# Performance work log

Hardware: AMD Instinct MI355X
Metric: run time of the kernel (lower is better)

The kernel has to match this reference:

```python
import jax, jax.numpy as jnp
import numpy as np

N, E, Q, D, R, K, L = 30000, 250000, 150000, 200, 400, 50, 2
ALPHA = 0.8   # TRIPLE_QUAL_WEIGHT
BN_EPS = 1e-5


def _rotate(h, r):
    # RotatE-style composition: complex mult with (re, im) = (first half, second half)
    hr, hi = jnp.split(h, 2, axis=-1)
    rr, ri = jnp.split(r, 2, axis=-1)
    return jnp.concatenate([hr * rr - hi * ri, hr * ri + hi * rr], axis=-1)


def _bn(x, g, b):
    # BatchNorm1d in training mode (batch statistics, biased variance)
    mu = x.mean(0)
    var = x.var(0)
    return g * (x - mu) * jax.lax.rsqrt(var + BN_EPS) + b


def _lrga(x, w, b):
    # LowRankAttention: shared Linear(d,4k)+ReLU then low-rank global attention
    t = jax.nn.relu(x @ w.T + b)                 # [N, 4K]
    U, V, Z, T = t[:, :K], t[:, K:2 * K], t[:, 2 * K:3 * K], t[:, 3 * K:]
    # joint_normalize2: scalar D = 1 / (sum(U @ (V^T @ 1)) / N + 1e-6)
    nf = jnp.sum(U @ (V.T @ jnp.ones((x.shape[0], 1), x.dtype))) / x.shape[0] + 1e-6
    return jnp.concatenate([(U @ (V.T @ Z)) / nf, T], axis=1)   # [N, 2K]


def _conv(x, rel, ei, et, qr, qe, qx, p):
    # StarEConvLayer forward (sparse qual mode, OPN=QUAL_OPN=rotate, no attention/bias)
    w_in, w_out, w_loop, w_rel, w_q, loop_rel, g, b = p
    n = x.shape[0]
    rel_all = jnp.concatenate([rel, loop_rel[None, :]], axis=0)  # [2R+2, d]

    def direction(idx, etype, qr_h, qe_h, qx_h, w):
        row, col = idx[0], idx[1]   # flow=target_to_source: gather col, scatter row
        deg = jax.ops.segment_sum(jnp.ones(row.shape, x.dtype), row, num_segments=n)
        dinv = jnp.where(deg > 0, deg ** -0.5, 0.0)
        norm = dinv[row] * dinv[col]
        # qualifier update of relation embedding per edge
        q_emb = _rotate(x[qe_h], rel_all[qr_h])                      # [Qh, d]
        q_edge = jax.ops.segment_sum(q_emb, qx_h, num_segments=E) @ w_q
        rel_e = ALPHA * rel_all[etype] + (1.0 - ALPHA) * q_edge     # [E, d]
        msg = (_rotate(x[col], rel_e) @ w) * norm[:, None]
        return jax.ops.segment_sum(msg, row, num_segments=n)

    in_res = direction(ei[:, :E], et[:E], qr[:Q], qe[:Q], qx[:Q], w_in)
    out_res = direction(ei[:, E:], et[E:], qr[Q:], qe[Q:], qx[Q:], w_out)
    loop_res = _rotate(x, rel_all[-1]) @ w_loop
    out = _bn((in_res + out_res + loop_res) / 3.0, g, b)
    return jax.nn.relu(out), (rel_all @ w_rel)[:-1]


def reference(edge_index, edge_type, quals_rel, quals_ent, quals_edge,
              ent_emb, init_rel, loop_rel, w_in, w_out, w_loop, w_rel, w_q,
              conv_gamma, conv_beta, lrga_w, lrga_b, dimred_w, dimred_b,
              fuse_gamma, fuse_beta):
    rev = jnp.stack([edge_index[1], edge_index[0]])
    ei = jnp.concatenate([edge_index, rev], axis=1)        # [2, 2E]
    et = jnp.concatenate([edge_type, edge_type + R])       # [2E]
    qr = jnp.concatenate([quals_rel, quals_rel])
    qe = jnp.concatenate([quals_ent, quals_ent])
    qx = jnp.concatenate([quals_edge, quals_edge])
    x, r = ent_emb, init_rel
    for i in range(L):
        p = (w_in[i], w_out[i], w_loop[i], w_rel[i], w_q[i], loop_rel[i],
             conv_gamma[i], conv_beta[i])
        x_local, r = _conv(x, r, ei, et, qr, qe, qx, p)
        x_global = _lrga(x, lrga_w[i], lrga_b[i])
        h = jnp.concatenate([x_global, x_local, x], axis=1) @ dimred_w[i].T + dimred_b[i]
        if i < L - 1:
            x = _bn(jax.nn.relu(h), fuse_gamma, fuse_beta)
        else:
            x = h
    return x, r


def setup_inputs():
    key = jax.random.key(0)
    ks = jax.random.split(key, 16)
    s = 1.0 / np.sqrt(D)
    return {
        "edge_index": jax.random.randint(ks[0], (2, E), 0, N, dtype=jnp.int32),
        "edge_type": jax.random.randint(ks[1], (E,), 0, R, dtype=jnp.int32),
        "quals_rel": jax.random.randint(ks[2], (Q,), 0, 2 * R, dtype=jnp.int32),
        "quals_ent": jax.random.randint(ks[3], (Q,), 0, N, dtype=jnp.int32),
        "quals_edge": jax.random.randint(ks[4], (Q,), 0, E, dtype=jnp.int32),
        "ent_emb": jax.random.normal(ks[5], (N, D)) * s,
        "init_rel": jax.random.normal(ks[6], (2 * R + 1, D)) * s,
        "loop_rel": jax.random.normal(ks[7], (L, D)) * s,
        "w_in": jax.random.normal(ks[8], (L, D, D)) * s,
        "w_out": jax.random.normal(ks[9], (L, D, D)) * s,
        "w_loop": jax.random.normal(ks[10], (L, D, D)) * s,
        "w_rel": jax.random.normal(ks[11], (L, D, D)) * s,
        "w_q": jax.random.normal(ks[12], (L, D, D)) * s,
        "conv_gamma": jnp.ones((L, D)),
        "conv_beta": jnp.zeros((L, D)),
        "lrga_w": jax.random.normal(ks[13], (L, 4 * K, D)) * s,
        "lrga_b": jnp.zeros((L, 4 * K)),
        "dimred_w": jax.random.normal(ks[14], (L, D, 2 * K + 2 * D)) * (1.0 / np.sqrt(2 * K + 2 * D)),
        "dimred_b": jnp.zeros((L, D)),
        "fuse_gamma": jnp.ones((D,)),
        "fuse_beta": jnp.zeros((D,)),
    }
```

## Files before the change

### kernel.cpp

```cpp
#include <hip/hip_runtime.h>
#include <cstdint>
#include <cstddef>

#define NN      30000
#define NE      250000
#define NQ      150000
#define DIM     200
#define DH      100
#define RRR     400
#define RELROWS 801
#define RELALL  802
#define ALPHA_C 0.8f
#define BN_EPS_C 1e-5f

__global__ void hist_kernel(const int* __restrict__ idx, int n, int* __restrict__ cnt) {
    int i = blockIdx.x * blockDim.x + threadIdx.x;
    if (i < n) atomicAdd(&cnt[idx[i]], 1);
}

#define SC_BLK 256
#define SC_PER 16
#define SC_TILE (SC_BLK * SC_PER)

__global__ __launch_bounds__(SC_BLK) void scan_blocks_kernel(
    const int* __restrict__ in, int n, int* __restrict__ out, int* __restrict__ partials)
{
    __shared__ int sh[SC_BLK];
    int b = blockIdx.x, tid = threadIdx.x;
    long base = (long)b * SC_TILE + (long)tid * SC_PER;
    int loc[SC_PER];
    int s = 0;
    #pragma unroll
    for (int j = 0; j < SC_PER; ++j) {
        long idx = base + j;
        int v = (idx < n) ? in[idx] : 0;
        loc[j] = s; s += v;
    }
    sh[tid] = s;
    __syncthreads();
    for (int o = 1; o < SC_BLK; o <<= 1) {
        int t = (tid >= o) ? sh[tid - o] : 0;
        __syncthreads();
        sh[tid] += t;
        __syncthreads();
    }
    int excl = sh[tid] - s;
    #pragma unroll
    for (int j = 0; j < SC_PER; ++j) {
        long idx = base + j;
        if (idx < n) out[idx] = excl + loc[j];
    }
    if (tid == SC_BLK - 1) partials[b] = sh[tid];
}

__global__ __launch_bounds__(1024) void scan_partials_kernel(
    int* __restrict__ partials, int np, int* __restrict__ out_total)
{
    __shared__ int sh[1024];
    int tid = threadIdx.x;
    int v = (tid < np) ? partials[tid] : 0;
    sh[tid] = v;
    __syncthreads();
    for (int o = 1; o < 1024; o <<= 1) {
        int t = (tid >= o) ? sh[tid - o] : 0;
        __syncthreads();
        sh[tid] += t;
        __syncthreads();
    }
    if (tid < np) partials[tid] = sh[tid] - v;
    if (tid == 1023) out_total[0] = sh[1023];
}

__global__ __launch_bounds__(SC_BLK) void scan_add_kernel(
    int* __restrict__ out, int n, const int* __restrict__ partials)
{
    int b = blockIdx.x;
    int add = partials[b];
    long base = (long)b * SC_TILE + threadIdx.x;
    #pragma unroll
    for (int j = 0; j < SC_PER; ++j) {
        long idx = base + (long)j * SC_BLK;
        if (idx < n) out[idx] += add;
    }
}

static inline void run_exscan(const int* in, int* out, int n, int* partials, hipStream_t s) {
    int nb = (n + SC_TILE - 1) / SC_TILE;
    scan_blocks_kernel<<<nb, SC_BLK, 0, s>>>(in, n, out, partials);
    scan_partials_kernel<<<1, 1024, 0, s>>>(partials, nb, out + n);
    scan_add_kernel<<<nb, SC_BLK, 0, s>>>(out, n, partials);
}

__global__ void scatter_kernel(const int* __restrict__ rows, int* __restrict__ cur,
                               int* __restrict__ list, int n) {
    int i = blockIdx.x * blockDim.x + threadIdx.x;
    if (i < n) {
        int r = rows[i];
        int pos = atomicAdd(&cur[r], 1);
        list[pos] = i;
    }
}

__global__ void dinv_kernel(const int* __restrict__ cnt, float* __restrict__ dinv, int n) {
    int i = blockIdx.x * blockDim.x + threadIdx.x;
    if (i < n) {
        int c = cnt[i];
        dinv[i] = (c > 0) ? 1.0f / sqrtf((float)c) : 0.0f;
    }
}

__global__ void assign_kernel(const int* __restrict__ qcnt, int* __restrict__ qidx,
                              int* __restrict__ elist, int* __restrict__ nq) {
    int e = blockIdx.x * blockDim.x + threadIdx.x;
    if (e < NE) {
        if (qcnt[e] > 0) {
            int s = atomicAdd(nq, 1);
            qidx[e] = s;
            elist[s] = e;
        } else {
            qidx[e] = -1;
        }
    }
}

__global__ __launch_bounds__(256) void qual_agg_kernel(
    const float* __restrict__ x, const float* __restrict__ rel_all,
    const int* __restrict__ qptr, const int* __restrict__ qlist,
    const int* __restrict__ qrel, const int* __restrict__ qent,
    const int* __restrict__ elist, const int* __restrict__ nq,
    float* __restrict__ qsum_c)
{
    int slot = blockIdx.x * 4 + (threadIdx.x >> 6);
    if (slot >= nq[0]) return;
    int e = elist[slot];
    int lane = threadIdx.x & 63;
    int p0 = lane;
    int p1 = lane + 64;
    bool has1 = (p1 < DH);
    float ar0 = 0.f, ai0 = 0.f, ar1 = 0.f, ai1 = 0.f;
    int s = qptr[e], t = qptr[e + 1];
    for (int i = s; i < t; ++i) {
        int q = qlist[i];
        int ent = qent[q];
        int rel = qrel[q];
        const float* xr = x + (long)ent * DIM;
        const float* rp = rel_all + (long)rel * DIM;
        {
            float hr = xr[p0], hi = xr[p0 + DH];
            float rr = rp[p0], ri = rp[p0 + DH];
            ar0 += hr * rr - hi * ri;
            ai0 += hr * ri + hi * rr;
        }
        if (has1) {
            float hr = xr[p1], hi = xr[p1 + DH];
            float rr = rp[p1], ri = rp[p1 + DH];
            ar1 += hr * rr - hi * ri;
            ai1 += hr * ri + hi * rr;
        }
    }
    float* o = qsum_c + (long)slot * DIM;
    o[p0] = ar0; o[p0 + DH] = ai0;
    if (has1) { o[p1] = ar1; o[p1 + DH] = ai1; }
}

__global__ __launch_bounds__(256) void edge_agg_kernel(
    const float* __restrict__ x, const float* __restrict__ rel_all,
    const float* __restrict__ q_edge_c, const int* __restrict__ qidx,
    const int* __restrict__ ptr, const int* __restrict__ list,
    const int* __restrict__ other, const int* __restrict__ etype,
    const float* __restrict__ dinv, int rel_off,
    float* __restrict__ out, int ldo, int col_off)
{
    int n = blockIdx.x * 4 + (threadIdx.x >> 6);
    if (n >= NN) return;
    int lane = threadIdx.x & 63;
    int p0 = lane;
    int p1 = lane + 64;
    bool has1 = (p1 < DH);
    float ar0 = 0.f, ai0 = 0.f, ar1 = 0.f, ai1 = 0.f;
    int s = ptr[n], e = ptr[n + 1];
    float dn = dinv[n];
    for (int i = s; i < e; ++i) {
        int eid = list[i];
        int col = other[eid];
        int t = etype[eid] + rel_off;
        int qi = qidx[eid];
        float norm = dn * dinv[col];
        const float* xr = x + (long)col * DIM;
        const float* rp = rel_all + (long)t * DIM;
        {
            float hr = xr[p0], hi = xr[p0 + DH];
            float wr = ALPHA_C * rp[p0];
            float wi = ALPHA_C * rp[p0 + DH];
            if (qi >= 0) {
                const float* qp = q_edge_c + (long)qi * DIM;
                wr += qp[p0]; wi += qp[p0 + DH];
            }
            ar0 += (hr * wr - hi * wi) * norm;
            ai0 += (hr * wi + hi * wr) * norm;
        }
        if (has1) {
            float hr = xr[p1], hi = xr[p1 + DH];
            float wr = ALPHA_C * rp[p1];
            float wi = ALPHA_C * rp[p1 + DH];
            if (qi >= 0) {
                const float* qp = q_edge_c + (long)qi * DIM;
                wr += qp[p1]; wi += qp[p1 + DH];
            }
            ar1 += (hr * wr - hi * wi) * norm;
            ai1 += (hr * wi + hi * wr) * norm;
        }
    }
    float* o = out + (long)n * ldo + col_off;
    o[p0] = ar0; o[p0 + DH] = ai0;
    if (has1) { o[p1] = ar1; o[p1 + DH] = ai1; }
}

__global__ __launch_bounds__(256) void rot_loop_kernel(
    const float* __restrict__ x, const float* __restrict__ rel_all,
    float* __restrict__ out, int ldo, int col_off)
{
    int n = blockIdx.x * 4 + (threadIdx.x >> 6);
    if (n >= NN) return;
    int lane = threadIdx.x & 63;
    const float* rp = rel_all + (long)(RELALL - 1) * DIM;
    const float* xr = x + (long)n * DIM;
    float* o = out + (long)n * ldo + col_off;
    {
        float hr = xr[lane], hi = xr[lane + DH];
        float rr = rp[lane], ri = rp[lane + DH];
        o[lane] = hr * rr - hi * ri;
        o[lane + DH] = hr * ri + hi * rr;
    }
    int p1 = lane + 64;
    if (p1 < DH) {
        float hr = xr[p1], hi = xr[p1 + DH];
        float rr = rp[p1], ri = rp[p1 + DH];
        o[p1] = hr * rr - hi * ri;
        o[p1 + DH] = hr * ri + hi * rr;
    }
}

__global__ void zero_kernel(float* __restrict__ p, long n) {
    long i = (long)blockIdx.x * blockDim.x + threadIdx.x;
    if (i < n) p[i] = 0.f;
}

#define BM 128
#define BN 128
#define BK 16

template <bool TRANSB>
__global__ __launch_bounds__(256) void gemm_kernel(
    const float* __restrict__ A, const float* __restrict__ B, float* __restrict__ C,
    int M, int K, int Ncols, int ldc,
    float scale, const float* __restrict__ bias, int relu, int acc,
    const int* __restrict__ Mdev)
{
    int Meff = Mdev ? Mdev[0] : M;
    int row0 = blockIdx.y * BM;
    if (row0 >= Meff) return;
    int col0 = blockIdx.x * BN;
    __shared__ float As[BK][BM + 4];
    __shared__ float Bs[BK][BN + 4];
    int tid = threadIdx.x;
    int tm = tid >> 4;
    int tn = tid & 15;
    float accv[8][8] = {{0.f}};
    int ktiles = (K + BK - 1) / BK;
    for (int kt = 0; kt < ktiles; ++kt) {
        int k0 = kt * BK;
        #pragma unroll
        for (int i = 0; i < 2; ++i) {
            int f4 = tid + i * 256;
            int m  = f4 >> 2;
            int kq = (f4 & 3) * 4;
            int gm = row0 + m, gk = k0 + kq;
            float4 v = make_float4(0.f, 0.f, 0.f, 0.f);
            if (gm < Meff) {
                if (gk + 3 < K) {
                    v = *reinterpret_cast<const float4*>(A + (long)gm * K + gk);
                } else {
                    float t0[4] = {0.f, 0.f, 0.f, 0.f};
                    #pragma unroll
                    for (int j = 0; j < 4; ++j) if (gk + j < K) t0[j] = A[(long)gm * K + gk + j];
                    v = make_float4(t0[0], t0[1], t0[2], t0[3]);
                }
            }
            As[kq + 0][m] = v.x; As[kq + 1][m] = v.y; As[kq + 2][m] = v.z; As[kq + 3][m] = v.w;
        }
        if (!TRANSB) {
            #pragma unroll
            for (int i = 0; i < 2; ++i) {
                int f4 = tid + i * 256;
                int k  = f4 >> 5;
                int n4 = (f4 & 31) * 4;
                int gk = k0 + k, gn = col0 + n4;
                float4 v = make_float4(0.f, 0.f, 0.f, 0.f);
                if (gk < K) {
                    if (gn + 3 < Ncols) {
                        v = *reinterpret_cast<const float4*>(B + (long)gk * Ncols + gn);
                    } else {
                        float t0[4] = {0.f, 0.f, 0.f, 0.f};
                        #pragma unroll
                        for (int j = 0; j < 4; ++j) if (gn + j < Ncols) t0[j] = B[(long)gk * Ncols + gn + j];
                        v = make_float4(t0[0], t0[1], t0[2], t0[3]);
                    }
                }
                Bs[k][n4 + 0] = v.x; Bs[k][n4 + 1] = v.y; Bs[k][n4 + 2] = v.z; Bs[k][n4 + 3] = v.w;
            }
        } else {
            #pragma unroll
            for (int i = 0; i < 2; ++i) {
                int f4 = tid + i * 256;
                int n  = f4 >> 2;
                int kq = (f4 & 3) * 4;
                int gn = col0 + n, gk = k0 + kq;
                float4 v = make_float4(0.f, 0.f, 0.f, 0.f);
                if (gn < Ncols) {
                    if (gk + 3 < K) {
                        v = *reinterpret_cast<const float4*>(B + (long)gn * K + gk);
                    } else {
                        float t0[4] = {0.f, 0.f, 0.f, 0.f};
                        #pragma unroll
                        for (int j = 0; j < 4; ++j) if (gk + j < K) t0[j] = B[(long)gn * K + gk + j];
                        v = make_float4(t0[0], t0[1], t0[2], t0[3]);
                    }
                }
                Bs[kq + 0][n] = v.x; Bs[kq + 1][n] = v.y; Bs[kq + 2][n] = v.z; Bs[kq + 3][n] = v.w;
            }
        }
        __syncthreads();
        #pragma unroll
        for (int k = 0; k < BK; ++k) {
            float a[8], b[8];
            #pragma unroll
            for (int i = 0; i < 8; ++i) a[i] = As[k][tm * 8 + i];
            #pragma unroll
            for (int j = 0; j < 8; ++j) b[j] = Bs[k][tn * 8 + j];
            #pragma unroll
            for (int i = 0; i < 8; ++i)
                #pragma unroll
                for (int j = 0; j < 8; ++j)
                    accv[i][j] += a[i] * b[j];
        }
        __syncthreads();
    }
    #pragma unroll
    for (int i = 0; i < 8; ++i) {
        int gm = row0 + tm * 8 + i;
        if (gm >= Meff) continue;
        #pragma unroll
        for (int j = 0; j < 8; ++j) {
            int gn = col0 + tn * 8 + j;
            if (gn >= Ncols) continue;
            float v = accv[i][j] * scale;
            if (bias) v += bias[gn];
            if (relu) v = fmaxf(v, 0.f);
            long off = (long)gm * ldc + gn;
            if (acc) v += C[off];
            C[off] = v;
        }
    }
}

__global__ __launch_bounds__(256) void bn_stats_kernel(
    const float* __restrict__ in, float scale, int relu_in,
    float* __restrict__ s1, float* __restrict__ s2)
{
    int d = threadIdx.x;
    if (d >= DIM) return;
    float a = 0.f, b = 0.f;
    for (int r = blockIdx.x; r < NN; r += gridDim.x) {
        float v = in[(long)r * DIM + d] * scale;
        if (relu_in) v = fmaxf(v, 0.f);
        a += v;
        b += v * v;
    }
    atomicAdd(&s1[d], a);
    atomicAdd(&s2[d], b);
}

__global__ void bn_finalize_kernel(
    const float* __restrict__ s1, const float* __restrict__ s2,
    const float* __restrict__ g, const float* __restrict__ be,
    float* __restrict__ aa, float* __restrict__ cc)
{
    int d = threadIdx.x;
    if (d >= DIM) return;
    float mu = s1[d] / (float)NN;
    float var = s2[d] / (float)NN - mu * mu;
    float inv = 1.0f / sqrtf(var + BN_EPS_C);
    float a = g[d] * inv;
    aa[d] = a;
    cc[d] = be[d] - mu * a;
}

__global__ __launch_bounds__(256) void bn_apply_kernel(
    const float* __restrict__ in, float scale, int relu_in,
    const float* __restrict__ aa, const float* __restrict__ cc, int relu_out,
    float* __restrict__ out, int ldo, int col0)
{
    int d = threadIdx.x;
    if (d >= DIM) return;
    int r = blockIdx.x;
    float v = in[(long)r * DIM + d] * scale;
    if (relu_in) v = fmaxf(v, 0.f);
    v = aa[d] * v + cc[d];
    if (relu_out) v = fmaxf(v, 0.f);
    out[(long)r * ldo + col0 + d] = v;
}

__global__ __launch_bounds__(128) void colsum_uv_kernel(
    const float* __restrict__ t, float* __restrict__ cs)
{
    int d = threadIdx.x;
    if (d >= 100) return;
    float s = 0.f;
    for (int r = blockIdx.x; r < NN; r += gridDim.x) s += t[(long)r * DIM + d];
    atomicAdd(&cs[d], s);
}

__global__ void nf_kernel(const float* __restrict__ cs, float* __restrict__ nf) {
    int lane = threadIdx.x;
    float v = (lane < 50) ? cs[lane] * cs[50 + lane] : 0.f;
    for (int off = 32; off > 0; off >>= 1) v += __shfl_down(v, off);
    if (lane == 0) nf[0] = v / (float)NN + 1e-6f;
}

__global__ __launch_bounds__(256) void vtz_kernel(
    const float* __restrict__ t, float* __restrict__ M50)
{
    __shared__ float vz[100];
    int tid = threadIdx.x;
    float acc[10];
    #pragma unroll
    for (int a = 0; a < 10; ++a) acc[a] = 0.f;
    for (int r = blockIdx.x; r < NN; r += gridDim.x) {
        if (tid < 100) vz[tid] = t[(long)r * DIM + 50 + tid];
        __syncthreads();
        #pragma unroll
        for (int a = 0; a < 10; ++a) {
            int p = tid + a * 256;
            if (p < 2500) {
                int i = p / 50, j = p % 50;
                acc[a] += vz[i] * vz[50 + j];
            }
        }
        __syncthreads();
    }
    #pragma unroll
    for (int a = 0; a < 10; ++a) {
        int p = tid + a * 256;
        if (p < 2500) atomicAdd(&M50[p], acc[a]);
    }
}

__global__ __launch_bounds__(256) void um_kernel(
    const float* __restrict__ t, const float* __restrict__ M50,
    const float* __restrict__ nf, float* __restrict__ cat)
{
    __shared__ float Ms[2500];
    int tid = threadIdx.x;
    for (int i = tid; i < 2500; i += 256) Ms[i] = M50[i];
    __syncthreads();
    int n = blockIdx.x * 256 + tid;
    if (n >= NN) return;
    float inv = 1.0f / nf[0];
    float acc[50];
    #pragma unroll
    for (int j = 0; j < 50; ++j) acc[j] = 0.f;
    for (int k = 0; k < 50; ++k) {
        float u = t[(long)n * DIM + k];
        #pragma unroll
        for (int j = 0; j < 50; ++j) acc[j] += u * Ms[k * 50 + j];
    }
    #pragma unroll
    for (int j = 0; j < 50; ++j) cat[(long)n * 500 + j] = acc[j] * inv;
}

__global__ __launch_bounds__(256) void copy_cols_kernel(
    const float* __restrict__ src, int lds_, int sc0,
    float* __restrict__ dst, int ldd, int dc0,
    int rows, int cols)
{
    int i = blockIdx.x * blockDim.x + threadIdx.x;
    int total = rows * cols;
    if (i >= total) return;
    int r = i / cols, c = i % cols;
    dst[(long)r * ldd + dc0 + c] = src[(long)r * lds_ + sc0 + c];
}

static inline void launch_gemm(bool transB, const float* A, const float* B, float* C,
                               int Mmax, int K, int Ncols, int ldc, float scale,
                               const float* bias, int relu, int acc,
                               const int* Mdev, hipStream_t s)
{
    dim3 grid((Ncols + BN - 1) / BN, (Mmax + BM - 1) / BM);
    if (transB)
        gemm_kernel<true><<<grid, 256, 0, s>>>(A, B, C, Mmax, K, Ncols, ldc, scale, bias, relu, acc, Mdev);
    else
        gemm_kernel<false><<<grid, 256, 0, s>>>(A, B, C, Mmax, K, Ncols, ldc, scale, bias, relu, acc, Mdev);
}

extern "C" void kernel_launch(void* const* d_in, const int* in_sizes, int n_in,
                              void* d_out, int out_size, void* d_ws, size_t ws_size,
                              hipStream_t stream)
{
    const int*   edge_index = (const int*)d_in[0];
    const int*   ei0        = edge_index;
    const int*   ei1        = edge_index + NE;
    const int*   edge_type  = (const int*)d_in[1];
    const int*   quals_rel  = (const int*)d_in[2];
    const int*   quals_ent  = (const int*)d_in[3];
    const int*   quals_edge = (const int*)d_in[4];
    const float* ent_emb    = (const float*)d_in[5];
    const float* init_rel   = (const float*)d_in[6];
    const float* loop_rel   = (const float*)d_in[7];
    const float* w_in       = (const float*)d_in[8];
    const float* w_out      = (const float*)d_in[9];
    const float* w_loop     = (const float*)d_in[10];
    const float* w_rel      = (const float*)d_in[11];
    const float* w_q        = (const float*)d_in[12];
    const float* conv_gamma = (const float*)d_in[13];
    const float* conv_beta  = (const float*)d_in[14];
    const float* lrga_w     = (const float*)d_in[15];
    const float* lrga_b     = (const float*)d_in[16];
    const float* dimred_w   = (const float*)d_in[17];
    const float* dimred_b   = (const float*)d_in[18];
    const float* fuse_gamma = (const float*)d_in[19];
    const float* fuse_beta  = (const float*)d_in[20];

    float* out_x = (float*)d_out;
    float* out_r = (float*)d_out + (long)NN * DIM;

    char* wp = (char*)d_ws;
    auto alloc = [&](size_t bytes) -> void* {
        void* p = (void*)wp;
        wp += (bytes + 255) & ~(size_t)255;
        return p;
    };
    float* regionA  = (float*)alloc(sizeof(float) * (size_t)NQ * DIM);
    float* qsum_c   = regionA;
    float* pre3     = regionA;
    float* conv_sum = regionA + (size_t)NN * 600;
    float* tbuf     = conv_sum + (size_t)NN * DIM;
    float* regionB  = (float*)alloc(sizeof(float) * (size_t)NQ * DIM);
    float* q_edge_c = regionB;
    float* cat      = regionB;
    float* hbuf     = cat + (size_t)NN * 500;
    float* x_cur    = out_x;
    float* rel_all  = (float*)alloc(sizeof(float) * (size_t)RELALL * DIM);
    float* r_buf    = (float*)alloc(sizeof(float) * (size_t)RELROWS * DIM);
    float* wcat     = (float*)alloc(sizeof(float) * 600 * DIM);
    float* dinv0    = (float*)alloc(sizeof(float) * NN);
    float* dinv1    = (float*)alloc(sizeof(float) * NN);
    float* s1       = (float*)alloc(sizeof(float) * DIM);
    float* s2       = (float*)alloc(sizeof(float) * DIM);
    float* aa       = (float*)alloc(sizeof(float) * DIM);
    float* cc       = (float*)alloc(sizeof(float) * DIM);
    float* csUV     = (float*)alloc(sizeof(float) * 100);
    float* nfv      = (float*)alloc(sizeof(float) * 1);
    float* M50      = (float*)alloc(sizeof(float) * 2500);
    int* cnt0  = (int*)alloc(sizeof(int) * NN);
    int* ptr0  = (int*)alloc(sizeof(int) * (NN + 1));
    int* cur0  = (int*)alloc(sizeof(int) * NN);
    int* list0 = (int*)alloc(sizeof(int) * NE);
    int* cnt1  = (int*)alloc(sizeof(int) * NN);
    int* ptr1  = (int*)alloc(sizeof(int) * (NN + 1));
    int* cur1  = (int*)alloc(sizeof(int) * NN);
    int* list1 = (int*)alloc(sizeof(int) * NE);
    int* qcnt  = (int*)alloc(sizeof(int) * NE);
    int* qptr  = (int*)alloc(sizeof(int) * (NE + 1));
    int* qcur  = (int*)alloc(sizeof(int) * NE);
    int* qlist = (int*)alloc(sizeof(int) * NQ);
    int* qidx  = (int*)alloc(sizeof(int) * NE);
    int* elist = (int*)alloc(sizeof(int) * NQ);
    int* nq    = (int*)alloc(sizeof(int) * 1);
    int* partials = (int*)alloc(sizeof(int) * 1024);

    size_t needed = (size_t)(wp - (char*)d_ws);
    if (needed > ws_size) {
        long total_out = (long)out_size;
        zero_kernel<<<(int)((total_out + 255) / 256), 256, 0, stream>>>((float*)d_out, total_out);
        return;
    }

    hipMemsetAsync(cnt0, 0, sizeof(int) * NN, stream);
    hipMemsetAsync(cnt1, 0, sizeof(int) * NN, stream);
    hipMemsetAsync(qcnt, 0, sizeof(int) * NE, stream);
    hipMemsetAsync(nq, 0, sizeof(int), stream);
    hist_kernel<<<(NE + 255) / 256, 256, 0, stream>>>(ei0, NE, cnt0);
    hist_kernel<<<(NE + 255) / 256, 256, 0, stream>>>(ei1, NE, cnt1);
    hist_kernel<<<(NQ + 255) / 256, 256, 0, stream>>>(quals_edge, NQ, qcnt);
    run_exscan(cnt0, ptr0, NN, partials, stream);
    run_exscan(cnt1, ptr1, NN, partials, stream);
    run_exscan(qcnt, qptr, NE, partials, stream);
    hipMemcpyAsync(cur0, ptr0, sizeof(int) * NN, hipMemcpyDeviceToDevice, stream);
    hipMemcpyAsync(cur1, ptr1, sizeof(int) * NN, hipMemcpyDeviceToDevice, stream);
    hipMemcpyAsync(qcur, qptr, sizeof(int) * NE, hipMemcpyDeviceToDevice, stream);
    scatter_kernel<<<(NE + 255) / 256, 256, 0, stream>>>(ei0, cur0, list0, NE);
    scatter_kernel<<<(NE + 255) / 256, 256, 0, stream>>>(ei1, cur1, list1, NE);
    scatter_kernel<<<(NQ + 255) / 256, 256, 0, stream>>>(quals_edge, qcur, qlist, NQ);
    dinv_kernel<<<(NN + 255) / 256, 256, 0, stream>>>(cnt0, dinv0, NN);
    dinv_kernel<<<(NN + 255) / 256, 256, 0, stream>>>(cnt1, dinv1, NN);
    assign_kernel<<<(NE + 255) / 256, 256, 0, stream>>>(qcnt, qidx, elist, nq);

    for (int i = 0; i < 2; ++i) {
        const float* xin  = (i == 0) ? ent_emb : x_cur;
        const float* rsrc = (i == 0) ? init_rel : r_buf;

        hipMemcpyAsync(rel_all, rsrc, sizeof(float) * RELROWS * DIM,
                       hipMemcpyDeviceToDevice, stream);
        hipMemcpyAsync(rel_all + (long)RELROWS * DIM, loop_rel + (long)i * DIM,
                       sizeof(float) * DIM, hipMemcpyDeviceToDevice, stream);

        qual_agg_kernel<<<(NQ + 3) / 4, 256, 0, stream>>>(xin, rel_all, qptr, qlist,
                                               quals_rel, quals_ent, elist, nq, qsum_c);
        launch_gemm(false, qsum_c, w_q + (long)i * DIM * DIM, q_edge_c,
                    NQ, DIM, DIM, DIM, 1.0f - ALPHA_C, nullptr, 0, 0, nq, stream);

        edge_agg_kernel<<<(NN + 3) / 4, 256, 0, stream>>>(xin, rel_all, q_edge_c, qidx,
                                               ptr0, list0, ei1, edge_type, dinv0, 0,
                                               pre3, 600, 0);
        edge_agg_kernel<<<(NN + 3) / 4, 256, 0, stream>>>(xin, rel_all, q_edge_c, qidx,
                                               ptr1, list1, ei0, edge_type, dinv1, RRR,
                                               pre3, 600, 200);
        rot_loop_kernel<<<(NN + 3) / 4, 256, 0, stream>>>(xin, rel_all, pre3, 600, 400);

        hipMemcpyAsync(wcat,                 w_in   + (long)i * DIM * DIM, sizeof(float) * DIM * DIM, hipMemcpyDeviceToDevice, stream);
        hipMemcpyAsync(wcat + DIM * DIM,     w_out  + (long)i * DIM * DIM, sizeof(float) * DIM * DIM, hipMemcpyDeviceToDevice, stream);
        hipMemcpyAsync(wcat + 2 * DIM * DIM, w_loop + (long)i * DIM * DIM, sizeof(float) * DIM * DIM, hipMemcpyDeviceToDevice, stream);
        launch_gemm(false, pre3, wcat, conv_sum, NN, 600, DIM, DIM, 1.f, nullptr, 0, 0, nullptr, stream);

        hipMemsetAsync(s1, 0, sizeof(float) * DIM, stream);
        hipMemsetAsync(s2, 0, sizeof(float) * DIM, stream);
        bn_stats_kernel<<<512, 256, 0, stream>>>(conv_sum, 1.0f / 3.0f, 0, s1, s2);
        bn_finalize_kernel<<<1, 256, 0, stream>>>(s1, s2, conv_gamma + (long)i * DIM,
                                                  conv_beta + (long)i * DIM, aa, cc);
        bn_apply_kernel<<<NN, 256, 0, stream>>>(conv_sum, 1.0f / 3.0f, 0, aa, cc, 1,
                                                cat, 500, 100);

        launch_gemm(true, xin, lrga_w + (long)i * 200 * DIM, tbuf,
                    NN, DIM, 200, 200, 1.f, lrga_b + (long)i * 200, 1, 0, nullptr, stream);
        hipMemsetAsync(csUV, 0, sizeof(float) * 100, stream);
        hipMemsetAsync(M50, 0, sizeof(float) * 2500, stream);
        colsum_uv_kernel<<<256, 128, 0, stream>>>(tbuf, csUV);
        nf_kernel<<<1, 64, 0, stream>>>(csUV, nfv);
        vtz_kernel<<<128, 256, 0, stream>>>(tbuf, M50);
        um_kernel<<<(NN + 255) / 256, 256, 0, stream>>>(tbuf, M50, nfv, cat);
        copy_cols_kernel<<<(NN * 50 + 255) / 256, 256, 0, stream>>>(
            tbuf, DIM, 150, cat, 500, 50, NN, 50);
        copy_cols_kernel<<<(NN * DIM + 255) / 256, 256, 0, stream>>>(
            xin, DIM, 0, cat, 500, 300, NN, DIM);

        float* hdst = (i == 0) ? hbuf : out_x;
        launch_gemm(true, cat, dimred_w + (long)i * DIM * 500, hdst,
                    NN, 500, DIM, DIM, 1.f, dimred_b + (long)i * DIM, 0, 0, nullptr, stream);

        if (i == 0) {
            hipMemsetAsync(s1, 0, sizeof(float) * DIM, stream);
            hipMemsetAsync(s2, 0, sizeof(float) * DIM, stream);
            bn_stats_kernel<<<512, 256, 0, stream>>>(hdst, 1.0f, 1, s1, s2);
            bn_finalize_kernel<<<1, 256, 0, stream>>>(s1, s2, fuse_gamma, fuse_beta, aa, cc);
            bn_apply_kernel<<<NN, 256, 0, stream>>>(hdst, 1.0f, 1, aa, cc, 0,
                                                    x_cur, DIM, 0);
        }

        float* rdst = (i == 0) ? r_buf : out_r;
        launch_gemm(false, rel_all, w_rel + (long)i * DIM * DIM, rdst,
                    RELROWS, DIM, DIM, DIM, 1.f, nullptr, 0, 0, nullptr, stream);
    }
}
```

Before: 2.529 ms.

## Double-buffer GEMM shared-memory tiles and vectorize LDS fragment reads

The FP32 SIMT GEMM now keeps two shared-memory buffers per operand. The next K-tile is prefetched into registers while the current tile is computed, which drops one barrier per iteration. The thread-to-output mapping changes to two strided 4-wide fragments, so each k-step reads shared memory with four float4 loads and fewer bank conflicts. This doubles LDS use and raises register pressure, which may reduce occupancy.

New measurement: 3.098 ms. 1.22x slower.

```diff
diff --git a/kernel.cpp b/kernel.cpp
--- a/kernel.cpp
+++ b/kernel.cpp
@@ -261,14 +261,17 @@
     int row0 = blockIdx.y * BM;
     if (row0 >= Meff) return;
     int col0 = blockIdx.x * BN;
-    __shared__ float As[BK][BM + 4];
-    __shared__ float Bs[BK][BN + 4];
+    __shared__ float As[2][BK][BM + 4];
+    __shared__ float Bs[2][BK][BN + 4];
     int tid = threadIdx.x;
     int tm = tid >> 4;
     int tn = tid & 15;
     float accv[8][8] = {{0.f}};
     int ktiles = (K + BK - 1) / BK;
-    for (int kt = 0; kt < ktiles; ++kt) {
+
+    float4 ra[2], rb[2];
+
+    auto loadA = [&](int kt) {
         int k0 = kt * BK;
         #pragma unroll
         for (int i = 0; i < 2; ++i) {
@@ -287,8 +290,11 @@
                     v = make_float4(t0[0], t0[1], t0[2], t0[3]);
                 }
             }
-            As[kq + 0][m] = v.x; As[kq + 1][m] = v.y; As[kq + 2][m] = v.z; As[kq + 3][m] = v.w;
-        }
+            ra[i] = v;
+        }
+    };
+    auto loadB = [&](int kt) {
+        int k0 = kt * BK;
         if (!TRANSB) {
             #pragma unroll
             for (int i = 0; i < 2; ++i) {
@@ -307,7 +313,7 @@
                         v = make_float4(t0[0], t0[1], t0[2], t0[3]);
                     }
                 }
-                Bs[k][n4 + 0] = v.x; Bs[k][n4 + 1] = v.y; Bs[k][n4 + 2] = v.z; Bs[k][n4 + 3] = v.w;
+                rb[i] = v;
             }
         } else {
             #pragma unroll
@@ -327,32 +333,74 @@
                         v = make_float4(t0[0], t0[1], t0[2], t0[3]);
                     }
                 }
-                Bs[kq + 0][n] = v.x; Bs[kq + 1][n] = v.y; Bs[kq + 2][n] = v.z; Bs[kq + 3][n] = v.w;
+                rb[i] = v;
             }
         }
+    };
+    auto storeA = [&](int buf) {
+        #pragma unroll
+        for (int i = 0; i < 2; ++i) {
+            int f4 = tid + i * 256;
+            int m  = f4 >> 2;
+            int kq = (f4 & 3) * 4;
+            As[buf][kq + 0][m] = ra[i].x; As[buf][kq + 1][m] = ra[i].y;
+            As[buf][kq + 2][m] = ra[i].z; As[buf][kq + 3][m] = ra[i].w;
+        }
+    };
+    auto storeB = [&](int buf) {
+        if (!TRANSB) {
+            #pragma unroll
+            for (int i = 0; i < 2; ++i) {
+                int f4 = tid + i * 256;
+                int k  = f4 >> 5;
+                int n4 = (f4 & 31) * 4;
+                Bs[buf][k][n4 + 0] = rb[i].x; Bs[buf][k][n4 + 1] = rb[i].y;
+                Bs[buf][k][n4 + 2] = rb[i].z; Bs[buf][k][n4 + 3] = rb[i].w;
+            }
+        } else {
+            #pragma unroll
+            for (int i = 0; i < 2; ++i) {
+                int f4 = tid + i * 256;
+                int n  = f4 >> 2;
+                int kq = (f4 & 3) * 4;
+                Bs[buf][kq + 0][n] = rb[i].x; Bs[buf][kq + 1][n] = rb[i].y;
+                Bs[buf][kq + 2][n] = rb[i].z; Bs[buf][kq + 3][n] = rb[i].w;
+            }
+        }
+    };
+
+    loadA(0); loadB(0);
+    storeA(0); storeB(0);
+    int cur = 0;
+
+    for (int kt = 0; kt < ktiles; ++kt) {
+        bool more = (kt + 1 < ktiles);
+        if (more) { loadA(kt + 1); loadB(kt + 1); }
         __syncthreads();
         #pragma unroll
         for (int k = 0; k < BK; ++k) {
             float a[8], b[8];
-            #pragma unroll
-            for (int i = 0; i < 8; ++i) a[i] = As[k][tm * 8 + i];
-            #pragma unroll
-            for (int j = 0; j < 8; ++j) b[j] = Bs[k][tn * 8 + j];
+            *reinterpret_cast<float4*>(&a[0]) = *reinterpret_cast<const float4*>(&As[cur][k][tm * 4]);
+            *reinterpret_cast<float4*>(&a[4]) = *reinterpret_cast<const float4*>(&As[cur][k][64 + tm * 4]);
+            *reinterpret_cast<float4*>(&b[0]) = *reinterpret_cast<const float4*>(&Bs[cur][k][tn * 4]);
+            *reinterpret_cast<float4*>(&b[4]) = *reinterpret_cast<const float4*>(&Bs[cur][k][64 + tn * 4]);
             #pragma unroll
             for (int i = 0; i < 8; ++i)
                 #pragma unroll
                 for (int j = 0; j < 8; ++j)
                     accv[i][j] += a[i] * b[j];
         }
-        __syncthreads();
-    }
+        if (more) { storeA(cur ^ 1); storeB(cur ^ 1); }
+        cur ^= 1;
+    }
+
     #pragma unroll
     for (int i = 0; i < 8; ++i) {
-        int gm = row0 + tm * 8 + i;
+        int gm = row0 + ((i < 4) ? (tm * 4 + i) : (64 + tm * 4 + (i - 4)));
         if (gm >= Meff) continue;
         #pragma unroll
         for (int j = 0; j < 8; ++j) {
-            int gn = col0 + tn * 8 + j;
+            int gn = col0 + ((j < 4) ? (tn * 4 + j) : (64 + tn * 4 + (j - 4)));
             if (gn >= Ncols) continue;
             float v = accv[i][j] * scale;
             if (bias) v += bias[gn];
```
